# Performance work log

Measured on AMD Instinct MI355X. Metric: run time of the kernel, lower is better.

## Reference

```python
import jax, jax.numpy as jnp
import numpy as np

PARTS = [[0, 1, 2, 3, 4], [5, 7, 9], [6, 8, 10], [11, 13, 15], [12, 14, 16]]
# joint i -> index of first part containing i (matches get_corr_joints)
JOINTS = np.array([0, 0, 0, 0, 0, 1, 2, 1, 2, 1, 2, 3, 4, 3, 4, 3, 4])
P = len(PARTS)
EPS = 1e-5


def _bn(y, g, b, m, v):
    # eval-mode BatchNorm2d over channel axis=1 of NCHW-like tensor
    scale = g / jnp.sqrt(v + EPS)
    return y * scale[None, :, None, None] + (b - m * scale)[None, :, None, None]


def setup_inputs() -> dict:
    C, Cq = 256, 64
    N, T, V = 64, 300, 17
    key = jax.random.key(0)
    ks = jax.random.split(key, 20)
    u = lambda k, s: jax.random.uniform(k, s, jnp.float32, 0.5, 1.5)
    n = lambda k, s: jax.random.normal(k, s, jnp.float32) * 0.1
    return {
        "x": jax.random.normal(ks[0], (N, C, T, V), jnp.float32),
        "part_w": n(ks[1], (P, Cq, C)),
        "part_b": n(ks[2], (P, Cq)),
        "pbn_g": u(ks[3], (P, Cq)),
        "pbn_b": n(ks[4], (P, Cq)),
        "pbn_m": n(ks[5], (P, Cq)),
        "pbn_v": u(ks[6], (P, Cq)),
        "fc1_w": n(ks[7], (Cq, Cq)),
        "fc1_b": n(ks[8], (Cq,)),
        "fbn_g": u(ks[9], (Cq,)),
        "fbn_b": n(ks[10], (Cq,)),
        "fbn_m": n(ks[11], (Cq,)),
        "fbn_v": u(ks[12], (Cq,)),
        "fc2_w": n(ks[13], (C * P, Cq)),
        "fc2_b": n(ks[14], (C * P,)),
        "bn_g": u(ks[15], (C,)),
        "bn_b": n(ks[16], (C,)),
        "bn_m": n(ks[17], (C,)),
        "bn_v": u(ks[18], (C,)),
    }


def reference(x, part_w, part_b, pbn_g, pbn_b, pbn_m, pbn_v,
              fc1_w, fc1_b, fbn_g, fbn_b, fbn_m, fbn_v,
              fc2_w, fc2_b, bn_g, bn_b, bn_m, bn_v):
    N, C, T, V = x.shape
    # per-part 1x1 conv + BN + ReLU + global average pool -> [N, Cq], summed over parts
    pooled = 0.0
    for p, idx in enumerate(PARTS):
        xp = x[:, :, :, np.array(idx)]                       # [N, C, T, k]
        y = jnp.einsum('nctv,qc->nqtv', xp, part_w[p]) + part_b[p][None, :, None, None]
        y = jax.nn.relu(_bn(y, pbn_g[p], pbn_b[p], pbn_m[p], pbn_v[p]))
        pooled = pooled + y.mean(axis=(2, 3))                # [N, Cq]
    # fcn: 1x1 conv + BN + ReLU + 1x1 conv (acting on [N, Cq, 1, 1])
    h = pooled @ fc1_w.T + fc1_b
    scale = fbn_g / jnp.sqrt(fbn_v + EPS)
    h = jax.nn.relu(h * scale + (fbn_b - fbn_m * scale))
    z = h @ fc2_w.T + fc2_b                                  # [N, C*P]
    att = jax.nn.softmax(z.reshape(N, C, P), axis=-1)        # [N, C, P]
    # gather attention per joint, broadcast over time
    att_v = att[:, :, JOINTS]                                # [N, C, V]
    out = x * att_v[:, :, None, :]
    return jax.nn.relu(_bn(out, bn_g, bn_b, bn_m, bn_v) + x)
```

## Files before the change

kernel.cpp:

```cpp
#include <hip/hip_runtime.h>
#include <hip/hip_bf16.h>


typedef __attribute__((ext_vector_type(8))) short short8;
typedef __attribute__((ext_vector_type(4))) float f32x4;
typedef float f4u __attribute__((ext_vector_type(4), aligned(4)));

__device__ __forceinline__ unsigned short f2bf(float f) {
    unsigned int u = __float_as_uint(f);
    u = (u + 0x7FFFu + ((u >> 16) & 1u)) >> 16;
    return (unsigned short)u;
}

__global__ void fold_kernel(
    const float* __restrict__ part_b, const float* __restrict__ pbn_g,
    const float* __restrict__ pbn_b,  const float* __restrict__ pbn_m,
    const float* __restrict__ pbn_v,
    const float* __restrict__ fc1_b,  const float* __restrict__ fbn_g,
    const float* __restrict__ fbn_b,  const float* __restrict__ fbn_m,
    const float* __restrict__ fbn_v,
    const float* __restrict__ bn_g,   const float* __restrict__ bn_b,
    const float* __restrict__ bn_m,   const float* __restrict__ bn_v,
    float* __restrict__ ps, float* __restrict__ pb,
    float* __restrict__ fs, float* __restrict__ fb,
    float* __restrict__ cs, float* __restrict__ cb)
{
    int tid = threadIdx.x;
    if (tid < 320) {
        float s = pbn_g[tid] * rsqrtf(pbn_v[tid] + 1e-5f);
        ps[tid] = s;
        pb[tid] = part_b[tid] * s + pbn_b[tid] - pbn_m[tid] * s;
    }
    if (tid < 64) {
        float s = fbn_g[tid] * rsqrtf(fbn_v[tid] + 1e-5f);
        fs[tid] = s;
        fb[tid] = fc1_b[tid] * s + fbn_b[tid] - fbn_m[tid] * s;
    }
    if (tid < 256) {
        float s = bn_g[tid] * rsqrtf(bn_v[tid] + 1e-5f);
        cs[tid] = s;
        cb[tid] = bn_b[tid] - bn_m[tid] * s;
    }
}

__global__ void conv_w_kernel(const float* __restrict__ pw, unsigned short* __restrict__ wq2)
{
    int i = blockIdx.x * 256 + threadIdx.x;
    if (i < 5 * 64 * 256) {
        int p = i >> 14;
        int q = (i >> 8) & 63;
        int c = i & 255;
        int kc = c >> 5, g = (c >> 3) & 3, j = c & 7;
        int wv = q >> 4, r15 = q & 15;
        wq2[((((p * 8 + kc) * 4 + wv) * 4 + g) * 16 + r15) * 8 + j] = f2bf(pw[i]);
    }
}

__global__ __launch_bounds__(256, 3) void part_pool_kernel(
    const float* __restrict__ x, const unsigned short* __restrict__ wq2,
    const float* __restrict__ ps, const float* __restrict__ pbs,
    float* __restrict__ pooled)
{
    constexpr int PMAP[17] = {0,0,0,0,0, 1,1,1, 2,2,2, 3,3,3, 4,4,4};
    constexpr int BASE[5]  = {0,80,128,176,224};
    constexpr int CNT[5]   = {5,3,3,3,3};
    constexpr float COEF[5] = {1.f/1500.f, 1.f/900.f, 1.f/900.f, 1.f/900.f, 1.f/900.f};

    __shared__ short Xn[32 * 272];
    __shared__ short Xt[272 * 32];
    __shared__ unsigned short rows4[68][4];

    const int tid  = threadIdx.x;
    const int lane = tid & 63;
    const int wv   = tid >> 6;
    const int r15  = lane & 15;
    const int g    = lane >> 4;

    const int blk = blockIdx.x;
    const int n   = blk / 19;
    const int tb  = (blk % 19) * 16;
    const bool tail = (tb + 16 > 300);

    if (tid < 68) {
        #pragma unroll
        for (int j = 0; j < 4; ++j) {
            const int f = 4 * tid + j;
            const int t = (int)(((unsigned)f * 61681u) >> 20);
            const int v = f - 17 * t;
            int row;
            if (v < 5)        row = v + 5 * t;
            else if (v < 11)  row = ((v & 1) ? (80 + ((v - 5) >> 1)) : (128 + ((v - 6) >> 1))) + 3 * t;
            else              row = ((v & 1) ? (176 + ((v - 11) >> 1)) : (224 + ((v - 12) >> 1))) + 3 * t;
            rows4[tid][j] = (unsigned short)row;
        }
    }

    f32x4 acc[17];
    #pragma unroll
    for (int m = 0; m < 17; ++m) acc[m] = (f32x4){0.f, 0.f, 0.f, 0.f};

    const size_t xbase = (size_t)n * 1305600 + (size_t)tb * 17;

    for (int cc = 0; cc < 256; cc += 32) {
        __syncthreads();

        #pragma unroll
        for (int it = 0; it < 9; ++it) {
            const int pi = it * 256 + tid;
            if (pi < 2176) {
                const int c = (int)(((unsigned)pi * 61681u) >> 22);
                const int q = pi - 68 * c;
                const float* gp = x + xbase + (size_t)(cc + c) * 5100 + 4 * q;
                unsigned int lo, hi2;
                if (!tail) {
                    f4u xv = *(const f4u*)gp;
                    lo  = (unsigned int)f2bf(xv[0]) | ((unsigned int)f2bf(xv[1]) << 16);
                    hi2 = (unsigned int)f2bf(xv[2]) | ((unsigned int)f2bf(xv[3]) << 16);
                } else {
                    float e[4];
                    #pragma unroll
                    for (int j = 0; j < 4; ++j) {
                        const int f = 4 * q + j;
                        const int t = (int)(((unsigned)f * 61681u) >> 20);
                        e[j] = 0.f;
                        if (tb + t < 300) e[j] = gp[j];
                    }
                    lo  = (unsigned int)f2bf(e[0]) | ((unsigned int)f2bf(e[1]) << 16);
                    hi2 = (unsigned int)f2bf(e[2]) | ((unsigned int)f2bf(e[3]) << 16);
                }
                *(uint2*)&Xn[c * 272 + 4 * q] = make_uint2(lo, hi2);
            }
        }
        __syncthreads();

        #pragma unroll
        for (int it = 0; it < 5; ++it) {
            const int pi = it * 256 + tid;
            if (pi < 1088) {
                const int cp = (int)(((unsigned)pi * 61681u) >> 22);
                const int q  = pi - 68 * cp;
                const uint2 a = *(const uint2*)&Xn[(2 * cp)     * 272 + 4 * q];
                const uint2 b = *(const uint2*)&Xn[(2 * cp + 1) * 272 + 4 * q];
                unsigned int w[4];
                w[0] = (a.x & 0xFFFFu) | (b.x << 16);
                w[1] = (a.x >> 16)     | (b.x & 0xFFFF0000u);
                w[2] = (a.y & 0xFFFFu) | (b.y << 16);
                w[3] = (a.y >> 16)     | (b.y & 0xFFFF0000u);
                const ushort4 rq = *(const ushort4*)&rows4[q][0];
                const int rr[4] = {rq.x, rq.y, rq.z, rq.w};
                #pragma unroll
                for (int j = 0; j < 4; ++j) {
                    const int row = rr[j];
                    const int off = row * 64 + ((cp * 4) ^ (((row >> 1) & 3) << 4));
                    *(unsigned int*)((char*)Xt + off) = w[j];
                }
            }
        }
        __syncthreads();

        const int kc = cc >> 5;
        short8 bfr[5];
        #pragma unroll
        for (int p = 0; p < 5; ++p)
            bfr[p] = *(const short8*)(wq2 + ((((p * 8 + kc) * 4 + wv) * 4 + g) * 16 + r15) * 8);

        #pragma unroll
        for (int m = 0; m < 17; ++m) {
            const int row = m * 16 + r15;
            const int off = row * 64 + ((g * 16) ^ (((row >> 1) & 3) << 4));
            short8 A = *(const short8*)((const char*)Xt + off);
            acc[m] = __builtin_amdgcn_mfma_f32_16x16x32_bf16(A, bfr[PMAP[m]], acc[m], 0, 0, 0);
        }
    }

    const int q = wv * 16 + r15;
    float s5[5], b5[5];
    #pragma unroll
    for (int p = 0; p < 5; ++p) { s5[p] = ps[(p << 6) + q]; b5[p] = pbs[(p << 6) + q]; }

    float sum = 0.f;
    #pragma unroll
    for (int m = 0; m < 17; ++m) {
        const int p = PMAP[m];
        #pragma unroll
        for (int rg = 0; rg < 4; ++rg) {
            const int row = m * 16 + g * 4 + rg;
            const int tl  = (row - BASE[p]) / CNT[p];
            if (tb + tl < 300) {
                float y = fmaf(s5[p], acc[m][rg], b5[p]);
                sum = fmaf(fmaxf(y, 0.f), COEF[p], sum);
            }
        }
    }
    sum += __shfl_xor(sum, 16);
    sum += __shfl_xor(sum, 32);
    if (g == 0) atomicAdd(&pooled[(n << 6) + q], sum);
}

__global__ __launch_bounds__(256) void fc_att_kernel(
    const float* __restrict__ pooled, const float* __restrict__ fc1_w,
    const float* __restrict__ fs, const float* __restrict__ fb,
    const float* __restrict__ fc2_w, const float* __restrict__ fc2_b,
    float* __restrict__ att)
{
    __shared__ float pl[64];
    __shared__ float hl[64];
    const int n = blockIdx.x;
    const int tid = threadIdx.x;

    if (tid < 64) pl[tid] = pooled[(n << 6) + tid];
    __syncthreads();
    if (tid < 64) {
        float d = 0.f;
        #pragma unroll
        for (int j = 0; j < 64; ++j) d = fmaf(pl[j], fc1_w[(tid << 6) + j], d);
        hl[tid] = fmaxf(fmaf(d, fs[tid], fb[tid]), 0.f);
    }
    __syncthreads();

    const int c = tid;
    float z[5];
    #pragma unroll
    for (int p = 0; p < 5; ++p) {
        const float* wrow = fc2_w + ((size_t)(c * 5 + p) << 6);
        float d = fc2_b[c * 5 + p];
        #pragma unroll
        for (int i = 0; i < 64; ++i) d = fmaf(hl[i], wrow[i], d);
        z[p] = d;
    }
    float m = z[0];
    #pragma unroll
    for (int p = 1; p < 5; ++p) m = fmaxf(m, z[p]);
    float e[5], ssum = 0.f;
    #pragma unroll
    for (int p = 0; p < 5; ++p) { e[p] = __expf(z[p] - m); ssum += e[p]; }
    const float inv = 1.f / ssum;
    #pragma unroll
    for (int p = 0; p < 5; ++p)
        att[((size_t)((n << 8) + c)) * 5 + p] = e[p] * inv;
}

__global__ __launch_bounds__(256) void apply_att_kernel(
    const float* __restrict__ x, const float* __restrict__ att,
    const float* __restrict__ cs, const float* __restrict__ cb,
    float* __restrict__ out)
{
    __shared__ float mult[17];
    const int nc  = blockIdx.x;
    const int c   = nc & 255;
    const int tid = threadIdx.x;

    if (tid < 17) {
        const int v = tid;
        const int p = (v < 5) ? 0 : ((v < 11) ? (2 - (v & 1)) : (4 - (v & 1)));
        mult[v] = fmaf(att[(size_t)nc * 5 + p], cs[c], 1.0f);
    }
    __syncthreads();

    const float cbc = cb[c];
    const float4* xp = (const float4*)(x + (size_t)nc * 5100);
    float4* op = (float4*)(out + (size_t)nc * 5100);

    for (int f = tid; f < 1275; f += 256) {
        float4 xv = xp[f];
        const int v0 = (4 * f) % 17;
        float o[4];
        const float xi[4] = {xv.x, xv.y, xv.z, xv.w};
        #pragma unroll
        for (int j = 0; j < 4; ++j) {
            int vj = v0 + j; if (vj >= 17) vj -= 17;
            o[j] = fmaxf(fmaf(xi[j], mult[vj], cbc), 0.f);
        }
        float4 ov; ov.x = o[0]; ov.y = o[1]; ov.z = o[2]; ov.w = o[3];
        op[f] = ov;
    }
}

extern "C" void kernel_launch(void* const* d_in, const int* in_sizes, int n_in,
                              void* d_out, int out_size, void* d_ws, size_t ws_size,
                              hipStream_t stream)
{
    const float* x      = (const float*)d_in[0];
    const float* part_w = (const float*)d_in[1];
    const float* part_b = (const float*)d_in[2];
    const float* pbn_g  = (const float*)d_in[3];
    const float* pbn_b  = (const float*)d_in[4];
    const float* pbn_m  = (const float*)d_in[5];
    const float* pbn_v  = (const float*)d_in[6];
    const float* fc1_w  = (const float*)d_in[7];
    const float* fc1_b  = (const float*)d_in[8];
    const float* fbn_g  = (const float*)d_in[9];
    const float* fbn_b  = (const float*)d_in[10];
    const float* fbn_m  = (const float*)d_in[11];
    const float* fbn_v  = (const float*)d_in[12];
    const float* fc2_w  = (const float*)d_in[13];
    const float* fc2_b  = (const float*)d_in[14];
    const float* bn_g   = (const float*)d_in[15];
    const float* bn_b   = (const float*)d_in[16];
    const float* bn_m   = (const float*)d_in[17];
    const float* bn_v   = (const float*)d_in[18];

    float* ws     = (float*)d_ws;
    float* pooled = ws;
    float* att    = ws + 4096;
    float* ps     = ws + 86016;
    float* pbias  = ws + 86336;
    float* fs     = ws + 86656;
    float* fb     = ws + 86720;
    float* cs     = ws + 86784;
    float* cb     = ws + 87040;
    unsigned short* wq2 = (unsigned short*)(ws + 87296);

    hipMemsetAsync(pooled, 0, 4096 * sizeof(float), stream);

    fold_kernel<<<1, 320, 0, stream>>>(part_b, pbn_g, pbn_b, pbn_m, pbn_v,
                                       fc1_b, fbn_g, fbn_b, fbn_m, fbn_v,
                                       bn_g, bn_b, bn_m, bn_v,
                                       ps, pbias, fs, fb, cs, cb);
    conv_w_kernel<<<320, 256, 0, stream>>>(part_w, wq2);
    part_pool_kernel<<<64 * 19, 256, 0, stream>>>(x, wq2, ps, pbias, pooled);
    fc_att_kernel<<<64, 256, 0, stream>>>(pooled, fc1_w, fs, fb, fc2_w, fc2_b, att);
    apply_att_kernel<<<16384, 256, 0, stream>>>(x, att, cs, cb, (float*)d_out);
}
```

Measured before the change: 285.7 us.

## Software-pipeline part-pool kernel with register prefetch and double-buffered LDS

Restructures the channel loop of the part-pool GEMM. Global loads for the next 32-channel chunk are issued into registers before the MFMA compute on the current chunk, and the transposed bf16 tile is double-buffered in LDS. The intermediate Xn staging buffer and one transpose pass are removed: each thread loads two channel rows and packs the bf16 pairs directly into the swizzled layout. The tail block handling switches to a per-slot bound, and the wide global loads now assume 16-byte alignment. In exchange the kernel holds more prefetch registers, which may lower occupancy under launch_bounds(256,3), and relies on hand-placed barriers and waitcnt.

Result: faster. 242.2 us (-15.2%).

```diff
diff --git a/kernel.cpp b/kernel.cpp
--- a/kernel.cpp
+++ b/kernel.cpp
@@ -4,7 +4,7 @@
 
 typedef __attribute__((ext_vector_type(8))) short short8;
 typedef __attribute__((ext_vector_type(4))) float f32x4;
-typedef float f4u __attribute__((ext_vector_type(4), aligned(4)));
+typedef float f4a __attribute__((ext_vector_type(4), aligned(16)));
 
 __device__ __forceinline__ unsigned short f2bf(float f) {
     unsigned int u = __float_as_uint(f);
@@ -66,8 +66,7 @@
     constexpr int CNT[5]   = {5,3,3,3,3};
     constexpr float COEF[5] = {1.f/1500.f, 1.f/900.f, 1.f/900.f, 1.f/900.f, 1.f/900.f};
 
-    __shared__ short Xn[32 * 272];
-    __shared__ short Xt[272 * 32];
+    __shared__ short Xt[2 * 272 * 32];
     __shared__ unsigned short rows4[68][4];
 
     const int tid  = threadIdx.x;
@@ -78,8 +77,8 @@
 
     const int blk = blockIdx.x;
     const int n   = blk / 19;
-    const int tb  = (blk % 19) * 16;
-    const bool tail = (tb + 16 > 300);
+    const int tb  = blk % 19;
+    const int fqmax = (tb == 18) ? 51 : 68;
 
     if (tid < 68) {
         #pragma unroll
@@ -94,86 +93,85 @@
             rows4[tid][j] = (unsigned short)row;
         }
     }
+    __syncthreads();
 
     f32x4 acc[17];
     #pragma unroll
     for (int m = 0; m < 17; ++m) acc[m] = (f32x4){0.f, 0.f, 0.f, 0.f};
 
-    const size_t xbase = (size_t)n * 1305600 + (size_t)tb * 17;
-
-    for (int cc = 0; cc < 256; cc += 32) {
-        __syncthreads();
-
-        #pragma unroll
-        for (int it = 0; it < 9; ++it) {
-            const int pi = it * 256 + tid;
-            if (pi < 2176) {
-                const int c = (int)(((unsigned)pi * 61681u) >> 22);
-                const int q = pi - 68 * c;
-                const float* gp = x + xbase + (size_t)(cc + c) * 5100 + 4 * q;
-                unsigned int lo, hi2;
-                if (!tail) {
-                    f4u xv = *(const f4u*)gp;
-                    lo  = (unsigned int)f2bf(xv[0]) | ((unsigned int)f2bf(xv[1]) << 16);
-                    hi2 = (unsigned int)f2bf(xv[2]) | ((unsigned int)f2bf(xv[3]) << 16);
-                } else {
-                    float e[4];
-                    #pragma unroll
-                    for (int j = 0; j < 4; ++j) {
-                        const int f = 4 * q + j;
-                        const int t = (int)(((unsigned)f * 61681u) >> 20);
-                        e[j] = 0.f;
-                        if (tb + t < 300) e[j] = gp[j];
-                    }
-                    lo  = (unsigned int)f2bf(e[0]) | ((unsigned int)f2bf(e[1]) << 16);
-                    hi2 = (unsigned int)f2bf(e[2]) | ((unsigned int)f2bf(e[3]) << 16);
-                }
-                *(uint2*)&Xn[c * 272 + 4 * q] = make_uint2(lo, hi2);
-            }
+    const size_t xrow = (size_t)n * 1305600 + (size_t)tb * 272;
+
+    f4a la[5], lb[5];
+
+    #define SLOTVARS(i) \
+        const int slot = (i) * 256 + tid; \
+        const int cp   = (int)((((unsigned)(slot >> 2)) * 61681u) >> 20); \
+        const int fq   = slot - 68 * cp; \
+        const bool ok  = (slot < 1088) && (fq < fqmax);
+
+    #define ISSUE(k) { \
+        const int cc_ = (k) * 32; \
+        _Pragma("unroll") \
+        for (int i = 0; i < 5; ++i) { \
+            SLOTVARS(i) \
+            if (ok) { \
+                const float* g0 = x + xrow + (size_t)(cc_ + 2 * cp) * 5100 + 4 * fq; \
+                la[i] = *(const f4a*)g0; \
+                lb[i] = *(const f4a*)(g0 + 5100); \
+            } \
+        } }
+
+    #define S1W(k) { \
+        char* xbuf = (char*)Xt + ((k) & 1) * 17408; \
+        _Pragma("unroll") \
+        for (int i = 0; i < 5; ++i) { \
+            SLOTVARS(i) \
+            if (ok) { \
+                const ushort4 rq = *(const ushort4*)&rows4[fq][0]; \
+                const int rr[4] = {rq.x, rq.y, rq.z, rq.w}; \
+                _Pragma("unroll") \
+                for (int j = 0; j < 4; ++j) { \
+                    const unsigned int pk = (unsigned int)f2bf(la[i][j]) \
+                                          | ((unsigned int)f2bf(lb[i][j]) << 16); \
+                    const int row = rr[j]; \
+                    const int off = row * 64 + ((cp * 4) ^ (((row >> 1) & 3) << 4)); \
+                    *(unsigned int*)(xbuf + off) = pk; \
+                } \
+            } \
+        } }
+
+    short8 wfr[5];
+    #define WFETCH(k) { \
+        _Pragma("unroll") \
+        for (int p = 0; p < 5; ++p) \
+            wfr[p] = *(const short8*)(wq2 + ((((p * 8 + (k)) * 4 + wv) * 4 + g) * 16 + r15) * 8); \
         }
-        __syncthreads();
-
-        #pragma unroll
-        for (int it = 0; it < 5; ++it) {
-            const int pi = it * 256 + tid;
-            if (pi < 1088) {
-                const int cp = (int)(((unsigned)pi * 61681u) >> 22);
-                const int q  = pi - 68 * cp;
-                const uint2 a = *(const uint2*)&Xn[(2 * cp)     * 272 + 4 * q];
-                const uint2 b = *(const uint2*)&Xn[(2 * cp + 1) * 272 + 4 * q];
-                unsigned int w[4];
-                w[0] = (a.x & 0xFFFFu) | (b.x << 16);
-                w[1] = (a.x >> 16)     | (b.x & 0xFFFF0000u);
-                w[2] = (a.y & 0xFFFFu) | (b.y << 16);
-                w[3] = (a.y >> 16)     | (b.y & 0xFFFF0000u);
-                const ushort4 rq = *(const ushort4*)&rows4[q][0];
-                const int rr[4] = {rq.x, rq.y, rq.z, rq.w};
-                #pragma unroll
-                for (int j = 0; j < 4; ++j) {
-                    const int row = rr[j];
-                    const int off = row * 64 + ((cp * 4) ^ (((row >> 1) & 3) << 4));
-                    *(unsigned int*)((char*)Xt + off) = w[j];
-                }
-            }
-        }
-        __syncthreads();
-
-        const int kc = cc >> 5;
-        short8 bfr[5];
-        #pragma unroll
-        for (int p = 0; p < 5; ++p)
-            bfr[p] = *(const short8*)(wq2 + ((((p * 8 + kc) * 4 + wv) * 4 + g) * 16 + r15) * 8);
-
-        #pragma unroll
-        for (int m = 0; m < 17; ++m) {
-            const int row = m * 16 + r15;
-            const int off = row * 64 + ((g * 16) ^ (((row >> 1) & 3) << 4));
-            short8 A = *(const short8*)((const char*)Xt + off);
-            acc[m] = __builtin_amdgcn_mfma_f32_16x16x32_bf16(A, bfr[PMAP[m]], acc[m], 0, 0, 0);
-        }
+
+    #define COMP(k) { \
+        const char* xbuf = (const char*)Xt + ((k) & 1) * 17408; \
+        _Pragma("unroll") \
+        for (int m = 0; m < 17; ++m) { \
+            const int row = m * 16 + r15; \
+            const int off = row * 64 + ((g * 16) ^ (((row >> 1) & 3) << 4)); \
+            short8 A = *(const short8*)(xbuf + off); \
+            acc[m] = __builtin_amdgcn_mfma_f32_16x16x32_bf16(A, wfr[PMAP[m]], acc[m], 0, 0, 0); \
+        } }
+
+    ISSUE(0);
+    for (int k = 0; k <= 8; ++k) {
+        if (k <= 7) S1W(k);
+        if (k >= 1) WFETCH(k - 1);
+        if (k <= 6) ISSUE(k + 1);
+        asm volatile("s_waitcnt lgkmcnt(0)" ::: "memory");
+        __builtin_amdgcn_s_barrier();
+        __builtin_amdgcn_sched_barrier(0);
+        if (k >= 1) COMP(k - 1);
+        __builtin_amdgcn_s_barrier();
+        __builtin_amdgcn_sched_barrier(0);
     }
 
     const int q = wv * 16 + r15;
+    const int tbt = tb * 16;
     float s5[5], b5[5];
     #pragma unroll
     for (int p = 0; p < 5; ++p) { s5[p] = ps[(p << 6) + q]; b5[p] = pbs[(p << 6) + q]; }
@@ -186,7 +184,7 @@
         for (int rg = 0; rg < 4; ++rg) {
             const int row = m * 16 + g * 4 + rg;
             const int tl  = (row - BASE[p]) / CNT[p];
-            if (tb + tl < 300) {
+            if (tbt + tl < 300) {
                 float y = fmaf(s5[p], acc[m][rg], b5[p]);
                 sum = fmaf(fmaxf(y, 0.f), COEF[p], sum);
             }
```
